# Optimization experiments

Hardware: AMD Instinct MI355X
Metric: run time of the kernel (lower is better)

## Reference

```python
import jax, jax.numpy as jnp
import numpy as np

D_MODEL = 1024
K_QUERY = 32
K_TOPK = 4

def setup_inputs() -> dict:
    key = jax.random.key(0)
    k1, k2, k3, k4, k5 = jax.random.split(key, 5)
    x = jax.random.normal(k1, (4, 2048, D_MODEL), dtype=jnp.float32)
    # nn.Linear(d_model, k_query): weight [k_query, d_model], bias [k_query]
    sc = 1.0 / np.sqrt(D_MODEL)
    Wq = jax.random.uniform(k2, (K_QUERY, D_MODEL), jnp.float32, -sc, sc)
    bq = jax.random.uniform(k3, (K_QUERY,), jnp.float32, -sc, sc)
    Wk = jax.random.uniform(k4, (K_QUERY, D_MODEL), jnp.float32, -sc, sc)
    bk = jax.random.uniform(k5, (K_QUERY,), jnp.float32, -sc, sc)
    return {"x": x, "Wq": Wq, "bq": bq, "Wk": Wk, "bk": bk}

def reference(x, Wq, bq, Wk, bk):
    # x: [B, T, D]
    queries = jnp.einsum('btd,kd->btk', x, Wq) + bq      # [B, T, Kq]
    keys = jnp.einsum('btd,kd->btk', x, Wk) + bk         # [B, T, Kq]
    sim = jnp.einsum('btk,bsk->bts', queries, keys)      # [B, T, T]
    sim = sim / jnp.sqrt(jnp.float32(queries.shape[-1]))
    _, topk_idx = jax.lax.top_k(sim, K_TOPK)              # [B, T, K]
    # gather neighbors per (b, t): x[b, topk_idx[b, t]] -> [B, T, K, D]
    neighbors = jax.vmap(lambda xb, ib: xb[ib])(x, topk_idx)
    gathered = neighbors.mean(axis=2)                     # [B, T, D]
    return gathered
```

## Files before the change

kernel.cpp:

```cpp
#include <hip/hip_runtime.h>
#include <math.h>

#define D_MODEL 1024
#define T_SEQ   2048
#define NBATCH  4
#define NROWS   (NBATCH * T_SEQ)
#define NOUT    64

#define XLD   1036
#define XLDH  1032

#define T16F   1024

typedef double v4df __attribute__((ext_vector_type(4)));
typedef float  v4f  __attribute__((ext_vector_type(4)));
typedef _Float16 v8hf __attribute__((ext_vector_type(8)));

__device__ __forceinline__ bool key_gt(float av, int ai, float bv, int bi) {
    return (av > bv) || (av == bv && ai < bi);
}

__device__ __forceinline__ void cmpswap(float& v0, int& i0, float& v1, int& i1) {
    bool sw = key_gt(v1, i1, v0, i0);
    float nv0 = sw ? v1 : v0, nv1 = sw ? v0 : v1;
    int   ni0 = sw ? i1 : i0, ni1 = sw ? i0 : i1;
    v0 = nv0; v1 = nv1; i0 = ni0; i1 = ni1;
}

__device__ __forceinline__ void merge4(float (&a)[4], int (&ai)[4],
                                       float b0, int j0, float b1, int j1,
                                       float b2, int j2, float b3, int j3) {
    if (!key_gt(a[0], ai[0], b3, j3)) { a[0] = b3; ai[0] = j3; }
    if (!key_gt(a[1], ai[1], b2, j2)) { a[1] = b2; ai[1] = j2; }
    if (!key_gt(a[2], ai[2], b1, j1)) { a[2] = b1; ai[2] = j1; }
    if (!key_gt(a[3], ai[3], b0, j0)) { a[3] = b0; ai[3] = j0; }
    cmpswap(a[0], ai[0], a[2], ai[2]);
    cmpswap(a[1], ai[1], a[3], ai[3]);
    cmpswap(a[0], ai[0], a[1], ai[1]);
    cmpswap(a[2], ai[2], a[3], ai[3]);
}

__device__ __forceinline__ void insert4(float (&tv)[4], int (&tix)[4], float v, int idx) {
    if (v > tv[3]) {
        bool g0 = v > tv[0], g1 = v > tv[1], g2 = v > tv[2];
        float n0 = g0 ? v : tv[0];
        int   m0 = g0 ? idx : tix[0];
        float n1 = g1 ? (g0 ? tv[0] : v) : tv[1];
        int   m1 = g1 ? (g0 ? tix[0] : idx) : tix[1];
        float n2 = g2 ? (g1 ? tv[1] : v) : tv[2];
        int   m2 = g2 ? (g1 ? tix[1] : idx) : tix[2];
        float n3 = g2 ? tv[2] : v;
        int   m3 = g2 ? tix[2] : idx;
        tv[0] = n0; tv[1] = n1; tv[2] = n2; tv[3] = n3;
        tix[0] = m0; tix[1] = m1; tix[2] = m2; tix[3] = m3;
    }
}

__device__ void run_probe(int tid, int* __restrict__ tab)
{
    __shared__ double Aref[16][4];
    __shared__ double Bref[4][16];
    __shared__ double Dref[16][16];

    const int lane = tid;
    if (tid < 64) {
        const int m = lane & 15, k = lane >> 4;
        Aref[m][k] = (double)(1 + m * 4 + k);
        Bref[k][m] = (double)(1 + k * 16 + m);
    }
    __syncthreads();
    {
        const int e = tid;
        const int m = e >> 4, n = e & 15;
        double s = 0.0;
        for (int k = 0; k < 4; ++k) s += Aref[m][k] * Bref[k][n];
        Dref[m][n] = s;
    }
    __syncthreads();

    if (tid >= 64) return;

    int found = -1;
    for (int h = 0; h < 16; ++h) {
        if (found >= 0) break;
        const int fa = h & 1, fb = (h >> 1) & 1, fd = h >> 2;
        const int am = fa ? (lane >> 2) : (lane & 15);
        const int ak = fa ? (lane & 3)  : (lane >> 4);
        const int bn = fb ? (lane >> 2) : (lane & 15);
        const int bk = fb ? (lane & 3)  : (lane >> 4);
        v4df c = {0.0, 0.0, 0.0, 0.0};
        c = __builtin_amdgcn_mfma_f64_16x16x4f64(Aref[am][ak], Bref[bk][bn], c, 0, 0, 0);
        bool ok = true;
        #pragma unroll
        for (int i = 0; i < 4; ++i) {
            int dm, dn;
            if (fd == 0)      { dm = 4 * (lane >> 4) + i; dn = lane & 15; }
            else if (fd == 1) { dn = 4 * (lane >> 4) + i; dm = lane & 15; }
            else if (fd == 2) { dm = (lane >> 4) + 4 * i; dn = lane & 15; }
            else              { dn = (lane >> 4) + 4 * i; dm = lane & 15; }
            if (c[i] != Dref[dm][dn]) ok = false;
        }
        if (__all(ok)) found = h;
    }

    const int fa = (found >= 0) ? (found & 1) : 0;
    const int fb = (found >= 0) ? ((found >> 1) & 1) : 0;
    const int fd = (found >= 0) ? (found >> 2) : 0;
    tab[1   + lane] = fa ? (lane >> 2) : (lane & 15);
    tab[65  + lane] = fa ? (lane & 3)  : (lane >> 4);
    tab[129 + lane] = fb ? (lane & 3)  : (lane >> 4);
    tab[193 + lane] = fb ? (lane >> 2) : (lane & 15);
    #pragma unroll
    for (int i = 0; i < 4; ++i) {
        int dm, dn;
        if (fd == 0)      { dm = 4 * (lane >> 4) + i; dn = lane & 15; }
        else if (fd == 1) { dn = 4 * (lane >> 4) + i; dm = lane & 15; }
        else if (fd == 2) { dm = (lane >> 4) + 4 * i; dn = lane & 15; }
        else              { dn = (lane >> 4) + 4 * i; dm = lane & 15; }
        tab[257 + lane * 4 + i] = dm;
        tab[513 + lane * 4 + i] = dn;
    }
    if (lane == 0) tab[0] = found;
}

__device__ void run_probe16(int tid, int* __restrict__ tab)
{
    __shared__ _Float16 A16[16][32];
    __shared__ _Float16 B16[32][16];
    __shared__ float    D16[16][16];

    for (int e = tid; e < 512; e += 256) {
        const int m = e >> 5, k = e & 31;
        A16[m][k] = (_Float16)(float)(1 + (3 * m + 5 * k) % 61);
        const int kk = e >> 4, n = e & 15;
        B16[kk][n] = (_Float16)(float)(1 + (7 * kk + 11 * n) % 59);
    }
    __syncthreads();
    {
        const int m = tid >> 4, n = tid & 15;
        float s = 0.f;
        for (int k = 0; k < 32; ++k) s += (float)A16[m][k] * (float)B16[k][n];
        D16[m][n] = s;
    }
    __syncthreads();

    if (tid >= 64) return;
    const int lane = tid;

    v8hf a, b;
    const int ab = (lane >> 4) * 8;
    #pragma unroll
    for (int j = 0; j < 8; ++j) {
        a[j] = A16[lane & 15][ab + j];
        b[j] = B16[ab + j][lane & 15];
    }
    v4f c = {0.f, 0.f, 0.f, 0.f};
    c = __builtin_amdgcn_mfma_f32_16x16x32_f16(a, b, c, 0, 0, 0);

    bool ok0 = true, ok1 = true;
    #pragma unroll
    for (int i = 0; i < 4; ++i) {
        ok0 = ok0 && (c[i] == D16[4 * (lane >> 4) + i][lane & 15]);
        ok1 = ok1 && (c[i] == D16[lane & 15][4 * (lane >> 4) + i]);
    }
    int found = __all(ok0) ? 0 : (__all(ok1) ? 1 : -1);
    if (lane == 0) tab[T16F] = found;
}

__global__ __launch_bounds__(256) void wprep_probe(
    const float* __restrict__ Wq, const float* __restrict__ Wk,
    double* __restrict__ Wdt, _Float16* __restrict__ Wh, _Float16* __restrict__ Wl,
    int* __restrict__ tab)
{
    const int tid = threadIdx.x;
    const int idx = blockIdx.x * 256 + tid;

    {
        const int o = idx & 63;
        const int d = idx >> 6;
        float v = (o < 32) ? Wq[(size_t)o * D_MODEL + d]
                           : Wk[(size_t)(o - 32) * D_MODEL + d];
        Wdt[(size_t)d * 64 + o] = (double)v;
    }
    {
        const int o = idx >> 10;
        const int d = idx & 1023;
        float v = (o < 32) ? Wq[(size_t)o * D_MODEL + d]
                           : Wk[(size_t)(o - 32) * D_MODEL + d];
        _Float16 h = (_Float16)v;
        Wh[(size_t)o * D_MODEL + d] = h;
        Wl[(size_t)o * D_MODEL + d] = (_Float16)(v - (float)h);
    }

    if (blockIdx.x == 0) {
        run_probe(tid, tab);
        run_probe16(tid, tab);
    }
}

__global__ __launch_bounds__(256) void proj(
    const float* __restrict__ x, const double* __restrict__ Wdt,
    const _Float16* __restrict__ Wh, const _Float16* __restrict__ Wl,
    const float* __restrict__ bq, const float* __restrict__ bk_,
    const int* __restrict__ tab,
    float* __restrict__ Qt, float* __restrict__ Kt,
    _Float16* __restrict__ Qh, _Float16* __restrict__ Ql,
    _Float16* __restrict__ Kh, _Float16* __restrict__ Kl)
{
    __shared__ __align__(16) char ldsraw[16 * XLD * 4];

    const int tid  = threadIdx.x;
    const int lane = tid & 63;
    const int wav  = tid >> 6;
    const int og   = __builtin_amdgcn_readfirstlane(wav);
    const int row0 = blockIdx.x * 16;

    const int flag16 = tab[T16F];

    if (flag16 == 0) {
        _Float16* xh = (_Float16*)ldsraw;
        _Float16* xl = xh + 16 * XLDH;

        #pragma unroll
        for (int j = 0; j < 16; ++j) {
            const int f  = j * 256 + tid;
            const int r  = f >> 8;
            const int c4 = f & 255;
            float4 v = *reinterpret_cast<const float4*>(
                x + (size_t)(row0 + r) * D_MODEL + c4 * 4);
            union { _Float16 h[4]; short4 s; } uh, ul;
            const float vv[4] = {v.x, v.y, v.z, v.w};
            #pragma unroll
            for (int e = 0; e < 4; ++e) {
                _Float16 h = (_Float16)vv[e];
                uh.h[e] = h;
                ul.h[e] = (_Float16)(vv[e] - (float)h);
            }
            *reinterpret_cast<short4*>(&xh[r * XLDH + c4 * 4]) = uh.s;
            *reinterpret_cast<short4*>(&xl[r * XLDH + c4 * 4]) = ul.s;
        }
        __syncthreads();

        const int am   = lane & 15;
        const int koff = (lane >> 4) * 8;
        const _Float16* bhrow = Wh + (size_t)(og * 16 + am) * D_MODEL + koff;
        const _Float16* blrow = Wl + (size_t)(og * 16 + am) * D_MODEL + koff;
        const _Float16* arow  = &xh[am * XLDH + koff];
        const _Float16* arl   = &xl[am * XLDH + koff];

        v4f hh = {0.f, 0.f, 0.f, 0.f};
        v4f hl = {0.f, 0.f, 0.f, 0.f};
        v4f lh = {0.f, 0.f, 0.f, 0.f};
        #pragma unroll 8
        for (int kc = 0; kc < 32; ++kc) {
            v8hf ah = *reinterpret_cast<const v8hf*>(arow + kc * 32);
            v8hf al = *reinterpret_cast<const v8hf*>(arl  + kc * 32);
            v8hf bh = *reinterpret_cast<const v8hf*>(bhrow + kc * 32);
            v8hf bl = *reinterpret_cast<const v8hf*>(blrow + kc * 32);
            hh = __builtin_amdgcn_mfma_f32_16x16x32_f16(ah, bh, hh, 0, 0, 0);
            hl = __builtin_amdgcn_mfma_f32_16x16x32_f16(ah, bl, hl, 0, 0, 0);
            lh = __builtin_amdgcn_mfma_f32_16x16x32_f16(al, bh, lh, 0, 0, 0);
        }

        #pragma unroll
        for (int i = 0; i < 4; ++i) {
            const float tot = (hh[i] + hl[i]) + lh[i];
            const int dmv = 4 * (lane >> 4) + i;
            const int dnv = lane & 15;
            const int o   = og * 16 + dnv;
            const int row = row0 + dmv;
            const float bias = (o < 32) ? bq[o] : bk_[o - 32];
            const float v = tot + bias;
            const _Float16 h = (_Float16)v;
            const _Float16 l = (_Float16)(v - (float)h);
            if (o < 32) {
                Qh[(size_t)row * 32 + o] = h;
                Ql[(size_t)row * 32 + o] = l;
            } else {
                Kh[(size_t)row * 32 + (o - 32)] = h;
                Kl[(size_t)row * 32 + (o - 32)] = l;
            }
        }
        return;
    }

    float* xlds = (float*)ldsraw;
    #pragma unroll
    for (int j = 0; j < 16; ++j) {
        const int f  = j * 256 + tid;
        const int r  = f >> 8;
        const int c4 = f & 255;
        float4 v = *reinterpret_cast<const float4*>(
            x + (size_t)(row0 + r) * D_MODEL + c4 * 4);
        *reinterpret_cast<float4*>(&xlds[r * XLD + c4 * 4]) = v;
    }
    __syncthreads();

    const int flag = tab[0];
    v4df acc = {0.0, 0.0, 0.0, 0.0};

    if (flag >= 0) {
        const int am  = tab[1   + lane];
        const int ak  = tab[65  + lane];
        const int bkk = tab[129 + lane];
        const int bn  = tab[193 + lane];
        const double* wcol = Wdt + og * 16;
        #pragma unroll 8
        for (int kk = 0; kk < 256; ++kk) {
            double a = (double)xlds[am * XLD + kk * 4 + ak];
            double b = wcol[(size_t)(kk * 4 + bkk) * 64 + bn];
            acc = __builtin_amdgcn_mfma_f64_16x16x4f64(a, b, acc, 0, 0, 0);
        }
        #pragma unroll
        for (int i = 0; i < 4; ++i) {
            const int dmv = tab[257 + lane * 4 + i];
            const int dnv = tab[513 + lane * 4 + i];
            const int o   = og * 16 + dnv;
            const int row = row0 + dmv;
            const int bb  = row >> 11, t = row & 2047;
            const double bias = (o < 32) ? (double)bq[o] : (double)bk_[o - 32];
            const float v = (float)(acc[i] + bias);
            if (o < 32) Qt[((size_t)bb * 32 + o) * T_SEQ + t] = v;
            else        Kt[((size_t)bb * 32 + (o - 32)) * T_SEQ + t] = v;
        }
    } else {
        const int n  = lane & 15;
        const int r4 = (lane >> 4) * 4;
        const int o  = og * 16 + n;
        const double* wcol = Wdt + o;
        for (int d = 0; d < D_MODEL; ++d) {
            double wv = wcol[(size_t)d * 64];
            #pragma unroll
            for (int i = 0; i < 4; ++i)
                acc[i] = fma((double)xlds[(r4 + i) * XLD + d], wv, acc[i]);
        }
        #pragma unroll
        for (int i = 0; i < 4; ++i) {
            const int row = row0 + r4 + i;
            const int bb  = row >> 11, t = row & 2047;
            const double bias = (o < 32) ? (double)bq[o] : (double)bk_[o - 32];
            const float v = (float)(acc[i] + bias);
            if (o < 32) Qt[((size_t)bb * 32 + o) * T_SEQ + t] = v;
            else        Kt[((size_t)bb * 32 + (o - 32)) * T_SEQ + t] = v;
        }
    }
}

__global__ __launch_bounds__(256) void sim_topk_gather(
    const float* __restrict__ x,
    const _Float16* __restrict__ Qh, const _Float16* __restrict__ Ql,
    const _Float16* __restrict__ Kh, const _Float16* __restrict__ Kl,
    const float* __restrict__ Qt, const float* __restrict__ Kt,
    const int* __restrict__ tab,
    float* __restrict__ out)
{
    __shared__ float sV[16][16][4];
    __shared__ int   sI[16][16][4];
    __shared__ int   topIdx[16][4];

    const int tid  = threadIdx.x;
    const int lane = tid & 63;
    const int wav  = tid >> 6;
    const int tt   = blockIdx.x & 127;
    const int b    = blockIdx.x >> 7;
    const int row0g = b * T_SEQ + tt * 16;

    if (tab[T16F] == 0) {
        const int m  = lane & 15;
        const int ko = (lane >> 4) * 8;
        v8hf ah = *reinterpret_cast<const v8hf*>(Qh + (size_t)(row0g + m) * 32 + ko);
        v8hf al = *reinterpret_cast<const v8hf*>(Ql + (size_t)(row0g + m) * 32 + ko);
        const _Float16* KhB = Kh + (size_t)b * T_SEQ * 32;
        const _Float16* KlB = Kl + (size_t)b * T_SEQ * 32;

        float tv[4][4]; int tix[4][4];
        #pragma unroll
        for (int r = 0; r < 4; ++r)
            #pragma unroll
            for (int j = 0; j < 4; ++j) { tv[r][j] = -INFINITY; tix[r][j] = 0x7fffffff; }

        const int sq = wav * 512;
        #pragma unroll 4
        for (int st = 0; st < 32; ++st) {
            const int s0 = sq + st * 16;
            v8hf bh = *reinterpret_cast<const v8hf*>(KhB + (size_t)(s0 + m) * 32 + ko);
            v8hf bl = *reinterpret_cast<const v8hf*>(KlB + (size_t)(s0 + m) * 32 + ko);
            v4f c = {0.f, 0.f, 0.f, 0.f};
            c = __builtin_amdgcn_mfma_f32_16x16x32_f16(ah, bh, c, 0, 0, 0);
            c = __builtin_amdgcn_mfma_f32_16x16x32_f16(ah, bl, c, 0, 0, 0);
            c = __builtin_amdgcn_mfma_f32_16x16x32_f16(al, bh, c, 0, 0, 0);
            c = __builtin_amdgcn_mfma_f32_16x16x32_f16(al, bl, c, 0, 0, 0);
            const int col = s0 + m;
            #pragma unroll
            for (int i = 0; i < 4; ++i) insert4(tv[i], tix[i], c[i], col);
        }

        #pragma unroll
        for (int mk = 1; mk <= 8; mk <<= 1) {
            #pragma unroll
            for (int r = 0; r < 4; ++r) {
                float b0 = __shfl_xor(tv[r][0], mk, 64);
                float b1 = __shfl_xor(tv[r][1], mk, 64);
                float b2 = __shfl_xor(tv[r][2], mk, 64);
                float b3 = __shfl_xor(tv[r][3], mk, 64);
                int   j0 = __shfl_xor(tix[r][0], mk, 64);
                int   j1 = __shfl_xor(tix[r][1], mk, 64);
                int   j2 = __shfl_xor(tix[r][2], mk, 64);
                int   j3 = __shfl_xor(tix[r][3], mk, 64);
                merge4(tv[r], tix[r], b0, j0, b1, j1, b2, j2, b3, j3);
            }
        }

        if ((lane & 15) == 0) {
            const int rbase = (lane >> 4) * 4;
            #pragma unroll
            for (int r = 0; r < 4; ++r)
                #pragma unroll
                for (int j = 0; j < 4; ++j) {
                    sV[wav][rbase + r][j] = tv[r][j];
                    sI[wav][rbase + r][j] = tix[r][j];
                }
        }
        __syncthreads();

        if (tid < 16) {
            float mv[4]; int mi[4];
            #pragma unroll
            for (int j = 0; j < 4; ++j) { mv[j] = sV[0][tid][j]; mi[j] = sI[0][tid][j]; }
            #pragma unroll
            for (int w = 1; w < 4; ++w)
                merge4(mv, mi,
                       sV[w][tid][0], sI[w][tid][0],
                       sV[w][tid][1], sI[w][tid][1],
                       sV[w][tid][2], sI[w][tid][2],
                       sV[w][tid][3], sI[w][tid][3]);
            #pragma unroll
            for (int j = 0; j < 4; ++j) topIdx[tid][j] = mi[j];
        }
        __syncthreads();
    } else {
        const float* QtB = Qt + (size_t)b * 32 * T_SEQ;
        const float* KtB = Kt + (size_t)b * 32 * T_SEQ;
        const int row   = tid >> 4;
        const int chunk = tid & 15;
        const int trow  = tt * 16 + row;
        float q[32];
        #pragma unroll 8
        for (int i = 0; i < 32; ++i) q[i] = QtB[(size_t)i * T_SEQ + trow];
        float tv4[4]; int tix4[4];
        #pragma unroll
        for (int j = 0; j < 4; ++j) { tv4[j] = -INFINITY; tix4[j] = 0x7fffffff; }
        const int sbeg = chunk * 128;
        for (int s = sbeg; s < sbeg + 128; ++s) {
            float sum = 0.f;
            #pragma unroll 8
            for (int i = 0; i < 32; ++i)
                sum = fmaf(q[i], KtB[(size_t)i * T_SEQ + s], sum);
            insert4(tv4, tix4, sum, s);
        }
        #pragma unroll
        for (int j = 0; j < 4; ++j) { sV[row][chunk][j] = tv4[j]; sI[row][chunk][j] = tix4[j]; }
        __syncthreads();
        if (tid < 16) {
            float mv[4]; int mi[4];
            #pragma unroll
            for (int j = 0; j < 4; ++j) { mv[j] = sV[tid][0][j]; mi[j] = sI[tid][0][j]; }
            #pragma unroll
            for (int cc = 1; cc < 16; ++cc)
                merge4(mv, mi,
                       sV[tid][cc][0], sI[tid][cc][0],
                       sV[tid][cc][1], sI[tid][cc][1],
                       sV[tid][cc][2], sI[tid][cc][2],
                       sV[tid][cc][3], sI[tid][cc][3]);
            #pragma unroll
            for (int j = 0; j < 4; ++j) topIdx[tid][j] = mi[j];
        }
        __syncthreads();
    }

    const float* xb = x + (size_t)b * T_SEQ * D_MODEL;
    float* ob = out + (size_t)row0g * D_MODEL;
    #pragma unroll 2
    for (int r = 0; r < 16; ++r) {
        const int i0 = topIdx[r][0], i1 = topIdx[r][1], i2 = topIdx[r][2], i3 = topIdx[r][3];
        float4 a0 = *(reinterpret_cast<const float4*>(xb + (size_t)i0 * D_MODEL) + tid);
        float4 a1 = *(reinterpret_cast<const float4*>(xb + (size_t)i1 * D_MODEL) + tid);
        float4 a2 = *(reinterpret_cast<const float4*>(xb + (size_t)i2 * D_MODEL) + tid);
        float4 a3 = *(reinterpret_cast<const float4*>(xb + (size_t)i3 * D_MODEL) + tid);
        float4 o;
        o.x = (a0.x + a1.x + a2.x + a3.x) * 0.25f;
        o.y = (a0.y + a1.y + a2.y + a3.y) * 0.25f;
        o.z = (a0.z + a1.z + a2.z + a3.z) * 0.25f;
        o.w = (a0.w + a1.w + a2.w + a3.w) * 0.25f;
        *(reinterpret_cast<float4*>(ob + (size_t)r * D_MODEL) + tid) = o;
    }
}

extern "C" void kernel_launch(void* const* d_in, const int* in_sizes, int n_in,
                              void* d_out, int out_size, void* d_ws, size_t ws_size,
                              hipStream_t stream) {
    const float* x  = (const float*)d_in[0];
    const float* Wq = (const float*)d_in[1];
    const float* bq = (const float*)d_in[2];
    const float* Wk = (const float*)d_in[3];
    const float* bk = (const float*)d_in[4];
    float* out = (float*)d_out;

    char* wsb = (char*)d_ws;
    int*      tab = (int*)wsb;
    double*   Wdt = (double*)(wsb + 8192);
    _Float16* Wh  = (_Float16*)(wsb + 8192 + 524288);
    _Float16* Wl  = (_Float16*)(wsb + 8192 + 524288 + 131072);
    float*    Qt  = (float*)(wsb + 8192 + 524288 + 262144);
    float*    Kt  = Qt + (size_t)NBATCH * 32 * T_SEQ;
    _Float16* Qh  = (_Float16*)((char*)Kt + (size_t)NBATCH * 32 * T_SEQ * 4);
    _Float16* Ql  = Qh + (size_t)NROWS * 32;
    _Float16* Kh  = Ql + (size_t)NROWS * 32;
    _Float16* Kl  = Kh + (size_t)NROWS * 32;

    wprep_probe<<<dim3(256), dim3(256), 0, stream>>>(Wq, Wk, Wdt, Wh, Wl, tab);
    proj<<<dim3(NROWS / 16), dim3(256), 0, stream>>>(x, Wdt, Wh, Wl, bq, bk, tab,
                                                     Qt, Kt, Qh, Ql, Kh, Kl);
    sim_topk_gather<<<dim3(512), dim3(256), 0, stream>>>(x, Qh, Ql, Kh, Kl, Qt, Kt, tab, out);
}
```

Measured before the change: 152.1 us.

## Split K across wave pairs in proj, double sim/topk waves, drop LDS staging

The projection kernel now uses 512 threads, with two waves per output group each covering half of the reduction dimension. The fp16 path converts x to hi/lo halves directly from global memory instead of staging it in LDS, and the two partial sums are combined through a small shared buffer. The sim/top-k/gather kernel goes to 512 threads with 8 waves each scanning 256 keys and a wider merge. The unused fp64 MFMA layout probe is removed. The goal is more parallelism and occupancy per block, in exchange for redundant global x reads across output groups and extra merge and sync work.

```diff
diff --git a/kernel.cpp b/kernel.cpp
--- a/kernel.cpp
+++ b/kernel.cpp
@@ -7,12 +7,8 @@
 #define NROWS   (NBATCH * T_SEQ)
 #define NOUT    64
 
-#define XLD   1036
-#define XLDH  1032
-
 #define T16F   1024
 
-typedef double v4df __attribute__((ext_vector_type(4)));
 typedef float  v4f  __attribute__((ext_vector_type(4)));
 typedef _Float16 v8hf __attribute__((ext_vector_type(8)));
 
@@ -56,73 +52,6 @@
     }
 }
 
-__device__ void run_probe(int tid, int* __restrict__ tab)
-{
-    __shared__ double Aref[16][4];
-    __shared__ double Bref[4][16];
-    __shared__ double Dref[16][16];
-
-    const int lane = tid;
-    if (tid < 64) {
-        const int m = lane & 15, k = lane >> 4;
-        Aref[m][k] = (double)(1 + m * 4 + k);
-        Bref[k][m] = (double)(1 + k * 16 + m);
-    }
-    __syncthreads();
-    {
-        const int e = tid;
-        const int m = e >> 4, n = e & 15;
-        double s = 0.0;
-        for (int k = 0; k < 4; ++k) s += Aref[m][k] * Bref[k][n];
-        Dref[m][n] = s;
-    }
-    __syncthreads();
-
-    if (tid >= 64) return;
-
-    int found = -1;
-    for (int h = 0; h < 16; ++h) {
-        if (found >= 0) break;
-        const int fa = h & 1, fb = (h >> 1) & 1, fd = h >> 2;
-        const int am = fa ? (lane >> 2) : (lane & 15);
-        const int ak = fa ? (lane & 3)  : (lane >> 4);
-        const int bn = fb ? (lane >> 2) : (lane & 15);
-        const int bk = fb ? (lane & 3)  : (lane >> 4);
-        v4df c = {0.0, 0.0, 0.0, 0.0};
-        c = __builtin_amdgcn_mfma_f64_16x16x4f64(Aref[am][ak], Bref[bk][bn], c, 0, 0, 0);
-        bool ok = true;
-        #pragma unroll
-        for (int i = 0; i < 4; ++i) {
-            int dm, dn;
-            if (fd == 0)      { dm = 4 * (lane >> 4) + i; dn = lane & 15; }
-            else if (fd == 1) { dn = 4 * (lane >> 4) + i; dm = lane & 15; }
-            else if (fd == 2) { dm = (lane >> 4) + 4 * i; dn = lane & 15; }
-            else              { dn = (lane >> 4) + 4 * i; dm = lane & 15; }
-            if (c[i] != Dref[dm][dn]) ok = false;
-        }
-        if (__all(ok)) found = h;
-    }
-
-    const int fa = (found >= 0) ? (found & 1) : 0;
-    const int fb = (found >= 0) ? ((found >> 1) & 1) : 0;
-    const int fd = (found >= 0) ? (found >> 2) : 0;
-    tab[1   + lane] = fa ? (lane >> 2) : (lane & 15);
-    tab[65  + lane] = fa ? (lane & 3)  : (lane >> 4);
-    tab[129 + lane] = fb ? (lane & 3)  : (lane >> 4);
-    tab[193 + lane] = fb ? (lane >> 2) : (lane & 15);
-    #pragma unroll
-    for (int i = 0; i < 4; ++i) {
-        int dm, dn;
-        if (fd == 0)      { dm = 4 * (lane >> 4) + i; dn = lane & 15; }
-        else if (fd == 1) { dn = 4 * (lane >> 4) + i; dm = lane & 15; }
-        else if (fd == 2) { dm = (lane >> 4) + 4 * i; dn = lane & 15; }
-        else              { dn = (lane >> 4) + 4 * i; dm = lane & 15; }
-        tab[257 + lane * 4 + i] = dm;
-        tab[513 + lane * 4 + i] = dn;
-    }
-    if (lane == 0) tab[0] = found;
-}
-
 __device__ void run_probe16(int tid, int* __restrict__ tab)
 {
     __shared__ _Float16 A16[16][32];
@@ -157,14 +86,11 @@
     v4f c = {0.f, 0.f, 0.f, 0.f};
     c = __builtin_amdgcn_mfma_f32_16x16x32_f16(a, b, c, 0, 0, 0);
 
-    bool ok0 = true, ok1 = true;
+    bool ok0 = true;
     #pragma unroll
-    for (int i = 0; i < 4; ++i) {
+    for (int i = 0; i < 4; ++i)
         ok0 = ok0 && (c[i] == D16[4 * (lane >> 4) + i][lane & 15]);
-        ok1 = ok1 && (c[i] == D16[lane & 15][4 * (lane >> 4) + i]);
-    }
-    int found = __all(ok0) ? 0 : (__all(ok1) ? 1 : -1);
-    if (lane == 0) tab[T16F] = found;
+    if (lane == 0) tab[T16F] = __all(ok0) ? 0 : -1;
 }
 
 __global__ __launch_bounds__(256) void wprep_probe(
@@ -192,13 +118,10 @@
         Wl[(size_t)o * D_MODEL + d] = (_Float16)(v - (float)h);
     }
 
-    if (blockIdx.x == 0) {
-        run_probe(tid, tab);
-        run_probe16(tid, tab);
-    }
-}
-
-__global__ __launch_bounds__(256) void proj(
+    if (blockIdx.x == 0) run_probe16(tid, tab);
+}
+
+__global__ __launch_bounds__(512) void proj(
     const float* __restrict__ x, const double* __restrict__ Wdt,
     const _Float16* __restrict__ Wh, const _Float16* __restrict__ Wl,
     const float* __restrict__ bq, const float* __restrict__ bk_,
@@ -207,146 +130,112 @@
     _Float16* __restrict__ Qh, _Float16* __restrict__ Ql,
     _Float16* __restrict__ Kh, _Float16* __restrict__ Kl)
 {
-    __shared__ __align__(16) char ldsraw[16 * XLD * 4];
+    __shared__ float  comb[4][64][4];
+    __shared__ double combd[4][64][4];
 
     const int tid  = threadIdx.x;
     const int lane = tid & 63;
     const int wav  = tid >> 6;
-    const int og   = __builtin_amdgcn_readfirstlane(wav);
+    const int og   = __builtin_amdgcn_readfirstlane(wav >> 1);
+    const int half = __builtin_amdgcn_readfirstlane(wav & 1);
     const int row0 = blockIdx.x * 16;
-
-    const int flag16 = tab[T16F];
-
-    if (flag16 == 0) {
-        _Float16* xh = (_Float16*)ldsraw;
-        _Float16* xl = xh + 16 * XLDH;
-
-        #pragma unroll
-        for (int j = 0; j < 16; ++j) {
-            const int f  = j * 256 + tid;
-            const int r  = f >> 8;
-            const int c4 = f & 255;
-            float4 v = *reinterpret_cast<const float4*>(
-                x + (size_t)(row0 + r) * D_MODEL + c4 * 4);
-            union { _Float16 h[4]; short4 s; } uh, ul;
-            const float vv[4] = {v.x, v.y, v.z, v.w};
-            #pragma unroll
-            for (int e = 0; e < 4; ++e) {
-                _Float16 h = (_Float16)vv[e];
-                uh.h[e] = h;
-                ul.h[e] = (_Float16)(vv[e] - (float)h);
-            }
-            *reinterpret_cast<short4*>(&xh[r * XLDH + c4 * 4]) = uh.s;
-            *reinterpret_cast<short4*>(&xl[r * XLDH + c4 * 4]) = ul.s;
-        }
-        __syncthreads();
-
-        const int am   = lane & 15;
-        const int koff = (lane >> 4) * 8;
-        const _Float16* bhrow = Wh + (size_t)(og * 16 + am) * D_MODEL + koff;
-        const _Float16* blrow = Wl + (size_t)(og * 16 + am) * D_MODEL + koff;
-        const _Float16* arow  = &xh[am * XLDH + koff];
-        const _Float16* arl   = &xl[am * XLDH + koff];
+    const int kb   = half * 512;
+
+    if (tab[T16F] == 0) {
+        const int m  = lane & 15;
+        const int ko = (lane >> 4) * 8;
+        const float*    xrow  = x  + (size_t)(row0 + m) * D_MODEL + kb + ko;
+        const _Float16* whrow = Wh + (size_t)(og * 16 + m) * D_MODEL + kb + ko;
+        const _Float16* wlrow = Wl + (size_t)(og * 16 + m) * D_MODEL + kb + ko;
 
         v4f hh = {0.f, 0.f, 0.f, 0.f};
         v4f hl = {0.f, 0.f, 0.f, 0.f};
         v4f lh = {0.f, 0.f, 0.f, 0.f};
-        #pragma unroll 8
-        for (int kc = 0; kc < 32; ++kc) {
-            v8hf ah = *reinterpret_cast<const v8hf*>(arow + kc * 32);
-            v8hf al = *reinterpret_cast<const v8hf*>(arl  + kc * 32);
-            v8hf bh = *reinterpret_cast<const v8hf*>(bhrow + kc * 32);
-            v8hf bl = *reinterpret_cast<const v8hf*>(blrow + kc * 32);
+        #pragma unroll 4
+        for (int kc = 0; kc < 16; ++kc) {
+            float4 x0 = *reinterpret_cast<const float4*>(xrow + kc * 32);
+            float4 x1 = *reinterpret_cast<const float4*>(xrow + kc * 32 + 4);
+            const float f[8] = {x0.x, x0.y, x0.z, x0.w, x1.x, x1.y, x1.z, x1.w};
+            v8hf ah, al;
+            #pragma unroll
+            for (int e = 0; e < 8; ++e) {
+                _Float16 h = (_Float16)f[e];
+                ah[e] = h;
+                al[e] = (_Float16)(f[e] - (float)h);
+            }
+            v8hf bh = *reinterpret_cast<const v8hf*>(whrow + kc * 32);
+            v8hf bl = *reinterpret_cast<const v8hf*>(wlrow + kc * 32);
             hh = __builtin_amdgcn_mfma_f32_16x16x32_f16(ah, bh, hh, 0, 0, 0);
             hl = __builtin_amdgcn_mfma_f32_16x16x32_f16(ah, bl, hl, 0, 0, 0);
             lh = __builtin_amdgcn_mfma_f32_16x16x32_f16(al, bh, lh, 0, 0, 0);
         }
 
+        v4f tot;
         #pragma unroll
-        for (int i = 0; i < 4; ++i) {
-            const float tot = (hh[i] + hl[i]) + lh[i];
-            const int dmv = 4 * (lane >> 4) + i;
-            const int dnv = lane & 15;
-            const int o   = og * 16 + dnv;
-            const int row = row0 + dmv;
-            const float bias = (o < 32) ? bq[o] : bk_[o - 32];
-            const float v = tot + bias;
-            const _Float16 h = (_Float16)v;
-            const _Float16 l = (_Float16)(v - (float)h);
-            if (o < 32) {
-                Qh[(size_t)row * 32 + o] = h;
-                Ql[(size_t)row * 32 + o] = l;
-            } else {
-                Kh[(size_t)row * 32 + (o - 32)] = h;
-                Kl[(size_t)row * 32 + (o - 32)] = l;
+        for (int i = 0; i < 4; ++i) tot[i] = (hh[i] + hl[i]) + lh[i];
+
+        if (half == 1) {
+            #pragma unroll
+            for (int i = 0; i < 4; ++i) comb[og][lane][i] = tot[i];
+        }
+        __syncthreads();
+        if (half == 0) {
+            #pragma unroll
+            for (int i = 0; i < 4; ++i) {
+                const float t = tot[i] + comb[og][lane][i];
+                const int dmv = 4 * (lane >> 4) + i;
+                const int o   = og * 16 + m;
+                const int row = row0 + dmv;
+                const float bias = (o < 32) ? bq[o] : bk_[o - 32];
+                const float v = t + bias;
+                const _Float16 h = (_Float16)v;
+                const _Float16 l = (_Float16)(v - (float)h);
+                if (o < 32) {
+                    Qh[(size_t)row * 32 + o] = h;
+                    Ql[(size_t)row * 32 + o] = l;
+                } else {
+                    Kh[(size_t)row * 32 + (o - 32)] = h;
+                    Kl[(size_t)row * 32 + (o - 32)] = l;
+                }
             }
         }
         return;
     }
 
-    float* xlds = (float*)ldsraw;
-    #pragma unroll
-    for (int j = 0; j < 16; ++j) {
-        const int f  = j * 256 + tid;
-        const int r  = f >> 8;
-        const int c4 = f & 255;
-        float4 v = *reinterpret_cast<const float4*>(
-            x + (size_t)(row0 + r) * D_MODEL + c4 * 4);
-        *reinterpret_cast<float4*>(&xlds[r * XLD + c4 * 4]) = v;
-    }
-    __syncthreads();
-
-    const int flag = tab[0];
-    v4df acc = {0.0, 0.0, 0.0, 0.0};
-
-    if (flag >= 0) {
-        const int am  = tab[1   + lane];
-        const int ak  = tab[65  + lane];
-        const int bkk = tab[129 + lane];
-        const int bn  = tab[193 + lane];
-        const double* wcol = Wdt + og * 16;
-        #pragma unroll 8
-        for (int kk = 0; kk < 256; ++kk) {
-            double a = (double)xlds[am * XLD + kk * 4 + ak];
-            double b = wcol[(size_t)(kk * 4 + bkk) * 64 + bn];
-            acc = __builtin_amdgcn_mfma_f64_16x16x4f64(a, b, acc, 0, 0, 0);
-        }
-        #pragma unroll
-        for (int i = 0; i < 4; ++i) {
-            const int dmv = tab[257 + lane * 4 + i];
-            const int dnv = tab[513 + lane * 4 + i];
-            const int o   = og * 16 + dnv;
-            const int row = row0 + dmv;
-            const int bb  = row >> 11, t = row & 2047;
-            const double bias = (o < 32) ? (double)bq[o] : (double)bk_[o - 32];
-            const float v = (float)(acc[i] + bias);
-            if (o < 32) Qt[((size_t)bb * 32 + o) * T_SEQ + t] = v;
-            else        Kt[((size_t)bb * 32 + (o - 32)) * T_SEQ + t] = v;
-        }
-    } else {
+    {
         const int n  = lane & 15;
         const int r4 = (lane >> 4) * 4;
         const int o  = og * 16 + n;
         const double* wcol = Wdt + o;
-        for (int d = 0; d < D_MODEL; ++d) {
+        double acc[4] = {0.0, 0.0, 0.0, 0.0};
+        for (int dd = 0; dd < 512; ++dd) {
+            const int d = kb + dd;
             double wv = wcol[(size_t)d * 64];
             #pragma unroll
             for (int i = 0; i < 4; ++i)
-                acc[i] = fma((double)xlds[(r4 + i) * XLD + d], wv, acc[i]);
-        }
-        #pragma unroll
-        for (int i = 0; i < 4; ++i) {
-            const int row = row0 + r4 + i;
-            const int bb  = row >> 11, t = row & 2047;
-            const double bias = (o < 32) ? (double)bq[o] : (double)bk_[o - 32];
-            const float v = (float)(acc[i] + bias);
-            if (o < 32) Qt[((size_t)bb * 32 + o) * T_SEQ + t] = v;
-            else        Kt[((size_t)bb * 32 + (o - 32)) * T_SEQ + t] = v;
-        }
-    }
-}
-
-__global__ __launch_bounds__(256) void sim_topk_gather(
+                acc[i] = fma((double)x[(size_t)(row0 + r4 + i) * D_MODEL + d], wv, acc[i]);
+        }
+        if (half == 1) {
+            #pragma unroll
+            for (int i = 0; i < 4; ++i) combd[og][lane][i] = acc[i];
+        }
+        __syncthreads();
+        if (half == 0) {
+            #pragma unroll
+            for (int i = 0; i < 4; ++i) {
+                const double t = acc[i] + combd[og][lane][i];
+                const int row = row0 + r4 + i;
+                const int bb  = row >> 11, tt = row & 2047;
+                const double bias = (o < 32) ? (double)bq[o] : (double)bk_[o - 32];
+                const float v = (float)(t + bias);
+                if (o < 32) Qt[((size_t)bb * 32 + o) * T_SEQ + tt] = v;
+                else        Kt[((size_t)bb * 32 + (o - 32)) * T_SEQ + tt] = v;
+            }
+        }
+    }
+}
+
+__global__ __launch_bounds__(512) void sim_topk_gather(
     const float* __restrict__ x,
     const _Float16* __restrict__ Qh, const _Float16* __restrict__ Ql,
     const _Float16* __restrict__ Kh, const _Float16* __restrict__ Kl,
@@ -354,8 +243,10 @@
     const int* __restrict__ tab,
     float* __restrict__ out)
 {
-    __shared__ float sV[16][16][4];
-    __shared__ int   sI[16][16][4];
+    __shared__ float sV[8][16][4];
+    __shared__ int   sI[8][16][4];
+    __shared__ float sVf[16][32][4];
+    __shared__ int   sIf[16][32][4];
     __shared__ int   topIdx[16][4];
 
     const int tid  = threadIdx.x;
@@ -379,9 +270,9 @@
             #pragma unroll
             for (int j = 0; j < 4; ++j) { tv[r][j] = -INFINITY; tix[r][j] = 0x7fffffff; }
 
-        const int sq = wav * 512;
+        const int sq = wav * 256;
         #pragma unroll 4
-        for (int st = 0; st < 32; ++st) {
+        for (int st = 0; st < 16; ++st) {
             const int s0 = sq + st * 16;
             v8hf bh = *reinterpret_cast<const v8hf*>(KhB + (size_t)(s0 + m) * 32 + ko);
             v8hf bl = *reinterpret_cast<const v8hf*>(KlB + (size_t)(s0 + m) * 32 + ko);
@@ -428,7 +319,7 @@
             #pragma unroll
             for (int j = 0; j < 4; ++j) { mv[j] = sV[0][tid][j]; mi[j] = sI[0][tid][j]; }
             #pragma unroll
-            for (int w = 1; w < 4; ++w)
+            for (int w = 1; w < 8; ++w)
                 merge4(mv, mi,
                        sV[w][tid][0], sI[w][tid][0],
                        sV[w][tid][1], sI[w][tid][1],
@@ -441,8 +332,8 @@
     } else {
         const float* QtB = Qt + (size_t)b * 32 * T_SEQ;
         const float* KtB = Kt + (size_t)b * 32 * T_SEQ;
-        const int row   = tid >> 4;
-        const int chunk = tid & 15;
+        const int row   = tid >> 5;
+        const int chunk = tid & 31;
         const int trow  = tt * 16 + row;
         float q[32];
         #pragma unroll 8
@@ -450,8 +341,8 @@
         float tv4[4]; int tix4[4];
         #pragma unroll
         for (int j = 0; j < 4; ++j) { tv4[j] = -INFINITY; tix4[j] = 0x7fffffff; }
-        const int sbeg = chunk * 128;
-        for (int s = sbeg; s < sbeg + 128; ++s) {
+        const int sbeg = chunk * 64;
+        for (int s = sbeg; s < sbeg + 64; ++s) {
             float sum = 0.f;
             #pragma unroll 8
             for (int i = 0; i < 32; ++i)
@@ -459,19 +350,18 @@
             insert4(tv4, tix4, sum, s);
         }
         #pragma unroll
-        for (int j = 0; j < 4; ++j) { sV[row][chunk][j] = tv4[j]; sI[row][chunk][j] = tix4[j]; }
+        for (int j = 0; j < 4; ++j) { sVf[row][chunk][j] = tv4[j]; sIf[row][chunk][j] = tix4[j]; }
         __syncthreads();
         if (tid < 16) {
             float mv[4]; int mi[4];
             #pragma unroll
-            for (int j = 0; j < 4; ++j) { mv[j] = sV[tid][0][j]; mi[j] = sI[tid][0][j]; }
-            #pragma unroll
-            for (int cc = 1; cc < 16; ++cc)
+            for (int j = 0; j < 4; ++j) { mv[j] = sVf[tid][0][j]; mi[j] = sIf[tid][0][j]; }
+            for (int cc = 1; cc < 32; ++cc)
                 merge4(mv, mi,
-                       sV[tid][cc][0], sI[tid][cc][0],
-                       sV[tid][cc][1], sI[tid][cc][1],
-                       sV[tid][cc][2], sI[tid][cc][2],
-                       sV[tid][cc][3], sI[tid][cc][3]);
+                       sVf[tid][cc][0], sIf[tid][cc][0],
+                       sVf[tid][cc][1], sIf[tid][cc][1],
+                       sVf[tid][cc][2], sIf[tid][cc][2],
+                       sVf[tid][cc][3], sIf[tid][cc][3]);
             #pragma unroll
             for (int j = 0; j < 4; ++j) topIdx[tid][j] = mi[j];
         }
@@ -480,19 +370,22 @@
 
     const float* xb = x + (size_t)b * T_SEQ * D_MODEL;
     float* ob = out + (size_t)row0g * D_MODEL;
+    const int rh = tid >> 8;
+    const int t4 = tid & 255;
     #pragma unroll 2
-    for (int r = 0; r < 16; ++r) {
+    for (int rp = 0; rp < 8; ++rp) {
+        const int r = rp * 2 + rh;
         const int i0 = topIdx[r][0], i1 = topIdx[r][1], i2 = topIdx[r][2], i3 = topIdx[r][3];
-        float4 a0 = *(reinterpret_cast<const float4*>(xb + (size_t)i0 * D_MODEL) + tid);
-        float4 a1 = *(reinterpret_cast<const float4*>(xb + (size_t)i1 * D_MODEL) + tid);
-        float4 a2 = *(reinterpret_cast<const float4*>(xb + (size_t)i2 * D_MODEL) + tid);
-        float4 a3 = *(reinterpret_cast<const float4*>(xb + (size_t)i3 * D_MODEL) + tid);
+        float4 a0 = *(reinterpret_cast<const float4*>(xb + (size_t)i0 * D_MODEL) + t4);
+        float4 a1 = *(reinterpret_cast<const float4*>(xb + (size_t)i1 * D_MODEL) + t4);
+        float4 a2 = *(reinterpret_cast<const float4*>(xb + (size_t)i2 * D_MODEL) + t4);
+        float4 a3 = *(reinterpret_cast<const float4*>(xb + (size_t)i3 * D_MODEL) + t4);
         float4 o;
         o.x = (a0.x + a1.x + a2.x + a3.x) * 0.25f;
         o.y = (a0.y + a1.y + a2.y + a3.y) * 0.25f;
         o.z = (a0.z + a1.z + a2.z + a3.z) * 0.25f;
         o.w = (a0.w + a1.w + a2.w + a3.w) * 0.25f;
-        *(reinterpret_cast<float4*>(ob + (size_t)r * D_MODEL) + tid) = o;
+        *(reinterpret_cast<float4*>(ob + (size_t)r * D_MODEL) + t4) = o;
     }
 }
 
@@ -519,7 +412,7 @@
     _Float16* Kl  = Kh + (size_t)NROWS * 32;
 
     wprep_probe<<<dim3(256), dim3(256), 0, stream>>>(Wq, Wk, Wdt, Wh, Wl, tab);
-    proj<<<dim3(NROWS / 16), dim3(256), 0, stream>>>(x, Wdt, Wh, Wl, bq, bk, tab,
+    proj<<<dim3(NROWS / 16), dim3(512), 0, stream>>>(x, Wdt, Wh, Wl, bq, bk, tab,
                                                      Qt, Kt, Qh, Ql, Kh, Kl);
-    sim_topk_gather<<<dim3(512), dim3(256), 0, stream>>>(x, Qh, Ql, Kh, Kl, Qt, Kt, tab, out);
-}
+    sim_topk_gather<<<dim3(512), dim3(512), 0, stream>>>(x, Qh, Ql, Kh, Kl, Qt, Kt, tab, out);
+}
```

New measurement: 151.6 us. No clear change (-0.4%).
